# Optimization experiments

Measured on AMD Instinct MI355X. Metric: run time of the kernel, lower is better.

## Reference

```python
import jax, jax.numpy as jnp
import numpy as np

N = 100000
IN_C = 256
OUT_C = 256
E = 500000


def gcn_conv(x, W, b, edges):
    """PyG GCNConv: add self-loops, symmetric D^-1/2 (A+I) D^-1/2 normalization,
    then scatter-add of transformed source features into targets, plus bias."""
    n = x.shape[0]
    loop = jnp.arange(n, dtype=edges.dtype)
    row = jnp.concatenate([edges[0], loop])  # source
    col = jnp.concatenate([edges[1], loop])  # target
    deg = jax.ops.segment_sum(jnp.ones_like(col, dtype=x.dtype), col, num_segments=n)
    dis = jax.lax.rsqrt(deg)  # deg >= 1 after self-loops
    norm = dis[row] * dis[col]  # [E+n]
    h = x @ W  # [n, out]
    msg = h[row] * norm[:, None]  # gather + scale
    return jax.ops.segment_sum(msg, col, num_segments=n) + b


def setup_inputs() -> dict:
    key = jax.random.key(0)
    ks = jax.random.split(key, 24)
    x = jax.random.normal(ks[0], (N, IN_C), dtype=jnp.float32)
    edges00 = jax.random.randint(ks[1], (2, E), 0, N, dtype=jnp.int32)
    edges01 = jax.random.randint(ks[2], (2, E), 0, N, dtype=jnp.int32)
    edges10 = jax.random.randint(ks[3], (2, E), 0, N, dtype=jnp.int32)
    edges11 = jax.random.randint(ks[4], (2, E), 0, N, dtype=jnp.int32)
    t0 = (jax.random.uniform(ks[5], (N,)) > 0.5).astype(jnp.float32)
    t1 = 1.0 - t0
    scale = 1.0 / np.sqrt(IN_C)
    W1 = jax.random.normal(ks[6], (IN_C, OUT_C), dtype=jnp.float32) * scale
    W2 = jax.random.normal(ks[7], (IN_C, OUT_C), dtype=jnp.float32) * scale
    W3 = jax.random.normal(ks[8], (IN_C, OUT_C), dtype=jnp.float32) * scale
    W4 = jax.random.normal(ks[9], (IN_C, OUT_C), dtype=jnp.float32) * scale
    b1 = jnp.zeros((OUT_C,), jnp.float32)
    b2 = jnp.zeros((OUT_C,), jnp.float32)
    b3 = jnp.zeros((OUT_C,), jnp.float32)
    b4 = jnp.zeros((OUT_C,), jnp.float32)
    p0 = jax.random.normal(ks[10], (OUT_C,), dtype=jnp.float32)
    p1 = jax.random.normal(ks[11], (OUT_C,), dtype=jnp.float32)
    p2 = jax.random.normal(ks[12], (OUT_C,), dtype=jnp.float32)
    p3 = jax.random.normal(ks[13], (OUT_C,), dtype=jnp.float32)
    p4 = jax.random.normal(ks[14], (OUT_C,), dtype=jnp.float32)
    p5 = jax.random.normal(ks[15], (OUT_C,), dtype=jnp.float32)
    return dict(x=x, edges00=edges00, edges01=edges01, edges10=edges10, edges11=edges11,
                type0_idx=t0, type1_idx=t1,
                W1=W1, b1=b1, W2=W2, b2=b2, W3=W3, b3=b3, W4=W4, b4=b4,
                p0=p0, p1=p1, p2=p2, p3=p3, p4=p4, p5=p5)


def reference(x, edges00, edges01, edges10, edges11, type0_idx, type1_idx,
              W1, b1, W2, b2, W3, b3, W4, b4, p0, p1, p2, p3, p4, p5):
    # x0/x1: first feature column masked by node type, broadcast over out channels
    x0c = type0_idx * x[:, 0]  # [N]
    x1c = type1_idx * x[:, 0]
    x00 = gcn_conv(x, W1, b1, edges00)
    x01 = gcn_conv(x, W2, b2, edges01)
    x10 = gcn_conv(x, W3, b3, edges10)
    x11 = gcn_conv(x, W4, b4, edges11)
    out = (x0c[:, None] * p0 + x1c[:, None] * p1
           + x00 * p2 + x01 * p3 + x10 * p4 + x11 * p5)
    return out
```

## Files before the change

kernel.cpp:

```cpp
#include <hip/hip_runtime.h>


typedef __bf16 v8bf __attribute__((ext_vector_type(8)));
typedef float v4f __attribute__((ext_vector_type(4)));

__device__ __forceinline__ unsigned short f2bf(float f) {
  unsigned u = __float_as_uint(f);
  u += 0x7fffu + ((u >> 16) & 1u);
  return (unsigned short)(u >> 16);
}
__device__ __forceinline__ float bf2f(unsigned short s) {
  return __uint_as_float(((unsigned)s) << 16);
}

__global__ void lc_zero(int* __restrict__ p, int n) {
  int i = blockIdx.x * 256 + threadIdx.x;
  if (i < n) p[i] = 0;
}

__global__ void lc_hist(const int* __restrict__ e0, const int* __restrict__ e1,
                        const int* __restrict__ e2, const int* __restrict__ e3,
                        int* __restrict__ hist, int N, int E) {
  int e = blockIdx.x * 256 + threadIdx.x;
  if (e >= E) return;
  int k = blockIdx.y;
  const int* ed = (k == 0) ? e0 : (k == 1) ? e1 : (k == 2) ? e2 : e3;
  int col = ed[E + e];
  atomicAdd(&hist[k * N + col], 1);
}

__global__ void lc_dis(const int* __restrict__ hist, float* __restrict__ dis, int M) {
  int i = blockIdx.x * 256 + threadIdx.x;
  if (i < M) dis[i] = rsqrtf((float)(hist[i] + 1));
}

__global__ void lc_scan1(const int* __restrict__ in, int* __restrict__ outp,
                         int* __restrict__ bsum, int M) {
  __shared__ int tmp[256];
  int t = threadIdx.x, i = blockIdx.x * 256 + t;
  int v = (i < M) ? in[i] : 0;
  tmp[t] = v;
  __syncthreads();
  for (int off = 1; off < 256; off <<= 1) {
    int add = (t >= off) ? tmp[t - off] : 0;
    __syncthreads();
    tmp[t] += add;
    __syncthreads();
  }
  if (i < M) outp[i] = tmp[t] - v;
  if (t == 255) bsum[blockIdx.x] = tmp[255];
}

__global__ void lc_scan2(int* __restrict__ bsum, int nb) {
  __shared__ int tmp[256];
  __shared__ int carry_s;
  int t = threadIdx.x;
  if (t == 0) carry_s = 0;
  __syncthreads();
  for (int base = 0; base < nb; base += 256) {
    int i = base + t;
    int v = (i < nb) ? bsum[i] : 0;
    tmp[t] = v;
    __syncthreads();
    for (int off = 1; off < 256; off <<= 1) {
      int add = (t >= off) ? tmp[t - off] : 0;
      __syncthreads();
      tmp[t] += add;
      __syncthreads();
    }
    int carry = carry_s;
    int total = tmp[255];
    if (i < nb) bsum[i] = carry + tmp[t] - v;
    __syncthreads();
    if (t == 0) carry_s = carry + total;
    __syncthreads();
  }
}

__global__ void lc_scan3(int* __restrict__ rp, int* __restrict__ cursor,
                         const int* __restrict__ bsum, int M) {
  int i = blockIdx.x * 256 + threadIdx.x;
  if (i < M) {
    int v = rp[i] + bsum[blockIdx.x];
    rp[i] = v;
    cursor[i] = v;
  }
}

__global__ void lc_fill(const int* __restrict__ e0, const int* __restrict__ e1,
                        const int* __restrict__ e2, const int* __restrict__ e3,
                        int* __restrict__ cursor, const float* __restrict__ dis,
                        int2* __restrict__ payload, int N, int E) {
  int e = blockIdx.x * 256 + threadIdx.x;
  if (e >= E) return;
  int k = blockIdx.y;
  const int* ed = (k == 0) ? e0 : (k == 1) ? e1 : (k == 2) ? e2 : e3;
  int src = ed[e], col = ed[E + e];
  int pos = atomicAdd(&cursor[k * N + col], 1);
  float nrm = dis[k * N + src] * dis[k * N + col];
  payload[pos] = make_int2(src, __float_as_int(nrm));
}

__global__ void lc_bias(const float* __restrict__ b1, const float* __restrict__ b2,
                        const float* __restrict__ b3, const float* __restrict__ b4,
                        const float* __restrict__ p2, const float* __restrict__ p3,
                        const float* __restrict__ p4, const float* __restrict__ p5,
                        float* __restrict__ biasc) {
  int c = threadIdx.x;
  biasc[c] = b1[c] * p2[c] + b2[c] * p3[c] + b3[c] * p4[c] + b4[c] * p5[c];
}

__global__ void lc_prep(const float* __restrict__ W1, const float* __restrict__ W2,
                        const float* __restrict__ W3, const float* __restrict__ W4,
                        const float* __restrict__ p2, const float* __restrict__ p3,
                        const float* __restrict__ p4, const float* __restrict__ p5,
                        unsigned short* __restrict__ Wt) {
  int b = blockIdx.x;
  int k = b >> 8, co = b & 255;
  int kk = threadIdx.x;
  const float* W = (k == 0) ? W1 : (k == 1) ? W2 : (k == 2) ? W3 : W4;
  const float* p = (k == 0) ? p2 : (k == 1) ? p3 : (k == 2) ? p4 : p5;
  Wt[(size_t)co * 1024 + k * 256 + kk] = f2bf(W[kk * 256 + co] * p[co]);
}

__global__ void lc_cvt(const float4* __restrict__ x4, ushort4* __restrict__ xb4,
                       const float* __restrict__ t0, const float* __restrict__ t1,
                       float* __restrict__ m0, float* __restrict__ m1, int n4) {
  int i = blockIdx.x * 256 + threadIdx.x;
  if (i >= n4) return;
  float4 v = x4[i];
  ushort4 r;
  r.x = f2bf(v.x); r.y = f2bf(v.y); r.z = f2bf(v.z); r.w = f2bf(v.w);
  xb4[i] = r;
  if ((i & 63) == 0) {
    int n = i >> 6;
    float xc = v.x;
    m0[n] = t0[n] * xc;
    m1[n] = t1[n] * xc;
  }
}

#define GAT1(POS, A0, A1, A2, A3)                                       \
  do {                                                                  \
    int2 ee = payload[POS];                                             \
    ushort4 gg = *(const ushort4*)&xb[(size_t)ee.x * 256 + c];          \
    float nn = __int_as_float(ee.y);                                    \
    A0 += bf2f(gg.x) * nn;                                              \
    A1 += bf2f(gg.y) * nn;                                              \
    A2 += bf2f(gg.z) * nn;                                              \
    A3 += bf2f(gg.w) * nn;                                              \
  } while (0)

__global__ __launch_bounds__(512, 4) void lc_fused(
    const unsigned short* __restrict__ xb, const unsigned short* __restrict__ Wt,
    const int* __restrict__ rp, const int* __restrict__ hist,
    const float* __restrict__ dis, const int2* __restrict__ payload,
    float* __restrict__ out, int N,
    const float* __restrict__ m0, const float* __restrict__ m1,
    const float* __restrict__ p0, const float* __restrict__ p1,
    const float* __restrict__ biasc) {
  __shared__ alignas(16) unsigned short As[32 * 1024];
  const int t = threadIdx.x;
  const int w = t >> 6, lane = t & 63;
  const int quad = lane >> 4, l16 = lane & 15;
  const int n0 = blockIdx.x * 32;
  const int c = lane * 4;

  for (int pb = 0; pb < 16; pb += 2) {
    int pr = w * 16 + pb;
    int ln = pr >> 2;
    int k0 = pr & 3;
    int n = n0 + ln;
    if (n >= N) n = N - 1;
    int idx0 = k0 * N + n;
    int idx1 = idx0 + N;
    float d0 = dis[idx0], d1 = dis[idx1];
    float s0v = d0 * d0, s1v = d1 * d1;
    ushort4 hv = *(const ushort4*)&xb[(size_t)n * 256 + c];
    float x0 = bf2f(hv.x), x1 = bf2f(hv.y), x2 = bf2f(hv.z), x3 = bf2f(hv.w);
    float a0 = x0 * s0v, a1 = x1 * s0v, a2 = x2 * s0v, a3 = x3 * s0v;
    float b0 = x0 * s1v, b1 = x1 * s1v, b2 = x2 * s1v, b3 = x3 * s1v;
    int st0 = rp[idx0], cnt0 = hist[idx0];
    int st1 = rp[idx1], cnt1 = hist[idx1];
    int i0 = 0, i1 = 0;
    while (i0 + 4 <= cnt0 && i1 + 4 <= cnt1) {
      GAT1(st0 + i0 + 0, a0, a1, a2, a3);
      GAT1(st0 + i0 + 1, a0, a1, a2, a3);
      GAT1(st0 + i0 + 2, a0, a1, a2, a3);
      GAT1(st0 + i0 + 3, a0, a1, a2, a3);
      GAT1(st1 + i1 + 0, b0, b1, b2, b3);
      GAT1(st1 + i1 + 1, b0, b1, b2, b3);
      GAT1(st1 + i1 + 2, b0, b1, b2, b3);
      GAT1(st1 + i1 + 3, b0, b1, b2, b3);
      i0 += 4;
      i1 += 4;
    }
    for (; i0 + 4 <= cnt0; i0 += 4) {
      GAT1(st0 + i0 + 0, a0, a1, a2, a3);
      GAT1(st0 + i0 + 1, a0, a1, a2, a3);
      GAT1(st0 + i0 + 2, a0, a1, a2, a3);
      GAT1(st0 + i0 + 3, a0, a1, a2, a3);
    }
    for (; i0 < cnt0; ++i0) GAT1(st0 + i0, a0, a1, a2, a3);
    for (; i1 + 4 <= cnt1; i1 += 4) {
      GAT1(st1 + i1 + 0, b0, b1, b2, b3);
      GAT1(st1 + i1 + 1, b0, b1, b2, b3);
      GAT1(st1 + i1 + 2, b0, b1, b2, b3);
      GAT1(st1 + i1 + 3, b0, b1, b2, b3);
    }
    for (; i1 < cnt1; ++i1) GAT1(st1 + i1, b0, b1, b2, b3);

    unsigned swz = (unsigned)((ln & 7) << 3);
    ushort4 r0, r1;
    r0.x = f2bf(a0); r0.y = f2bf(a1); r0.z = f2bf(a2); r0.w = f2bf(a3);
    r1.x = f2bf(b0); r1.y = f2bf(b1); r1.z = f2bf(b2); r1.w = f2bf(b3);
    *(ushort4*)&As[(unsigned)ln * 1024 + (((unsigned)(k0 * 256 + c)) ^ swz)] = r0;
    *(ushort4*)&As[(unsigned)ln * 1024 + (((unsigned)((k0 + 1) * 256 + c)) ^ swz)] = r1;
  }
  __syncthreads();

  v4f acc[2][2];
#pragma unroll
  for (int mt = 0; mt < 2; mt++)
#pragma unroll
    for (int nt = 0; nt < 2; nt++) {
      v4f z = {0.f, 0.f, 0.f, 0.f};
      acc[mt][nt] = z;
    }

  const unsigned short* Bp = Wt + (size_t)(w * 32 + l16) * 1024 + quad * 8;
#pragma unroll 4
  for (int kk = 0; kk < 1024; kk += 32) {
    int eq = (kk + quad * 8) ^ ((l16 & 7) << 3);
    v8bf af0 = *(const v8bf*)&As[(unsigned)l16 * 1024 + eq];
    v8bf af1 = *(const v8bf*)&As[(unsigned)(l16 + 16) * 1024 + eq];
    v8bf bq0 = *(const v8bf*)&Bp[kk];
    v8bf bq1 = *(const v8bf*)&Bp[16384 + kk];
    acc[0][0] = __builtin_amdgcn_mfma_f32_16x16x32_bf16(af0, bq0, acc[0][0], 0, 0, 0);
    acc[0][1] = __builtin_amdgcn_mfma_f32_16x16x32_bf16(af0, bq1, acc[0][1], 0, 0, 0);
    acc[1][0] = __builtin_amdgcn_mfma_f32_16x16x32_bf16(af1, bq0, acc[1][0], 0, 0, 0);
    acc[1][1] = __builtin_amdgcn_mfma_f32_16x16x32_bf16(af1, bq1, acc[1][1], 0, 0, 0);
  }

  float pc0[2], pc1[2], bcv[2];
#pragma unroll
  for (int nt = 0; nt < 2; nt++) {
    int gcol = w * 32 + nt * 16 + l16;
    pc0[nt] = p0[gcol];
    pc1[nt] = p1[gcol];
    bcv[nt] = biasc[gcol];
  }
#pragma unroll
  for (int mt = 0; mt < 2; mt++)
#pragma unroll
    for (int r = 0; r < 4; r++) {
      int grow = n0 + mt * 16 + quad * 4 + r;
      if (grow >= N) continue;
      float m0v = m0[grow], m1v = m1[grow];
#pragma unroll
      for (int nt = 0; nt < 2; nt++) {
        int gcol = w * 32 + nt * 16 + l16;
        out[(size_t)grow * 256 + gcol] =
            acc[mt][nt][r] + m0v * pc0[nt] + m1v * pc1[nt] + bcv[nt];
      }
    }
}

extern "C" void kernel_launch(void* const* d_in, const int* in_sizes, int n_in,
                              void* d_out, int out_size, void* d_ws, size_t ws_size,
                              hipStream_t stream) {
  const float* x = (const float*)d_in[0];
  const int* e00 = (const int*)d_in[1];
  const int* e01 = (const int*)d_in[2];
  const int* e10 = (const int*)d_in[3];
  const int* e11 = (const int*)d_in[4];
  const float* t0 = (const float*)d_in[5];
  const float* t1 = (const float*)d_in[6];
  const float* W1 = (const float*)d_in[7];
  const float* b1 = (const float*)d_in[8];
  const float* W2 = (const float*)d_in[9];
  const float* b2 = (const float*)d_in[10];
  const float* W3 = (const float*)d_in[11];
  const float* b3 = (const float*)d_in[12];
  const float* W4 = (const float*)d_in[13];
  const float* b4 = (const float*)d_in[14];
  const float* p0 = (const float*)d_in[15];
  const float* p1 = (const float*)d_in[16];
  const float* p2 = (const float*)d_in[17];
  const float* p3 = (const float*)d_in[18];
  const float* p4 = (const float*)d_in[19];
  const float* p5 = (const float*)d_in[20];
  float* out = (float*)d_out;

  int N = in_sizes[0] / 256;
  int E = in_sizes[1] / 2;
  int M4 = 4 * N;
  int nb = (M4 + 255) / 256;

  char* wp = (char*)d_ws;
  auto carve = [&](size_t bytes) {
    void* r = (void*)wp;
    wp += (bytes + 255) & ~(size_t)255;
    return r;
  };
  unsigned short* xb = (unsigned short*)carve((size_t)N * 256 * 2);
  unsigned short* Wt = (unsigned short*)carve((size_t)256 * 1024 * 2);
  int* hist = (int*)carve((size_t)M4 * 4);
  float* dis = (float*)carve((size_t)M4 * 4);
  int* rp = (int*)carve((size_t)M4 * 4);
  int* cursor = (int*)carve((size_t)M4 * 4);
  int* bsum = (int*)carve((size_t)nb * 4);
  float* biasc = (float*)carve(256 * 4);
  float* m0 = (float*)carve((size_t)N * 4);
  float* m1 = (float*)carve((size_t)N * 4);
  int2* payload = (int2*)carve((size_t)4 * E * 8);

  int gE = (E + 255) / 256;
  int gM = (M4 + 255) / 256;

  lc_zero<<<gM, 256, 0, stream>>>(hist, M4);
  lc_hist<<<dim3(gE, 4), 256, 0, stream>>>(e00, e01, e10, e11, hist, N, E);
  lc_dis<<<gM, 256, 0, stream>>>(hist, dis, M4);
  lc_scan1<<<nb, 256, 0, stream>>>(hist, rp, bsum, M4);
  lc_scan2<<<1, 256, 0, stream>>>(bsum, nb);
  lc_scan3<<<nb, 256, 0, stream>>>(rp, cursor, bsum, M4);
  lc_fill<<<dim3(gE, 4), 256, 0, stream>>>(e00, e01, e10, e11, cursor, dis, payload, N, E);
  lc_bias<<<1, 256, 0, stream>>>(b1, b2, b3, b4, p2, p3, p4, p5, biasc);
  lc_prep<<<1024, 256, 0, stream>>>(W1, W2, W3, W4, p2, p3, p4, p5, Wt);
  lc_cvt<<<(N * 64 + 255) / 256, 256, 0, stream>>>((const float4*)x, (ushort4*)xb,
                                                   t0, t1, m0, m1, N * 64);

  lc_fused<<<dim3((N + 31) / 32), 512, 0, stream>>>(xb, Wt, rp, hist, dis, payload,
                                                    out, N, m0, m1, p0, p1, biasc);
}
```

Measured before the change: 821.3 us.

## Halve shared memory via two-phase K split and predicate gather loop for occupancy

The fused gather+GEMM kernel now processes the four edge-type relations in two halves of K=512. Each half is gathered into a 32KB shared tile and consumed by MFMA before the next, which halves LDS use and raises the launch-bounds occupancy target from 4 to 8. The gather loops are merged into one predicated loop over the longer neighbor list, clamping indices and zeroing weights to avoid divergent tail loops. Warps are also remapped to a 2x4 grid with 4 N-tiles each. Risks include an extra barrier, wasted predicated loads when the two degree counts differ, and register pressure under the tighter bound.

After: 1.033 ms. +25.7%, slower.

```diff
diff --git a/kernel.cpp b/kernel.cpp
--- a/kernel.cpp
+++ b/kernel.cpp
@@ -140,18 +140,19 @@
   }
 }
 
-#define GAT1(POS, A0, A1, A2, A3)                                       \
+#define GATC(BASE, POS, LIM, CNT, A0, A1, A2, A3)                       \
   do {                                                                  \
-    int2 ee = payload[POS];                                             \
+    int jj = ((POS) < (CNT)) ? (POS) : (LIM);                           \
+    int2 ee = payload[(BASE) + jj];                                     \
     ushort4 gg = *(const ushort4*)&xb[(size_t)ee.x * 256 + c];          \
-    float nn = __int_as_float(ee.y);                                    \
+    float nn = ((POS) < (CNT)) ? __int_as_float(ee.y) : 0.f;            \
     A0 += bf2f(gg.x) * nn;                                              \
     A1 += bf2f(gg.y) * nn;                                              \
     A2 += bf2f(gg.z) * nn;                                              \
     A3 += bf2f(gg.w) * nn;                                              \
   } while (0)
 
-__global__ __launch_bounds__(512, 4) void lc_fused(
+__global__ __launch_bounds__(512, 8) void lc_fused(
     const unsigned short* __restrict__ xb, const unsigned short* __restrict__ Wt,
     const int* __restrict__ rp, const int* __restrict__ hist,
     const float* __restrict__ dis, const int2* __restrict__ payload,
@@ -159,111 +160,96 @@
     const float* __restrict__ m0, const float* __restrict__ m1,
     const float* __restrict__ p0, const float* __restrict__ p1,
     const float* __restrict__ biasc) {
-  __shared__ alignas(16) unsigned short As[32 * 1024];
+  __shared__ alignas(16) unsigned short As[32 * 512];
   const int t = threadIdx.x;
   const int w = t >> 6, lane = t & 63;
   const int quad = lane >> 4, l16 = lane & 15;
+  const int wr = w >> 2, wc = w & 3;
   const int n0 = blockIdx.x * 32;
   const int c = lane * 4;
 
-  for (int pb = 0; pb < 16; pb += 2) {
-    int pr = w * 16 + pb;
-    int ln = pr >> 2;
-    int k0 = pr & 3;
-    int n = n0 + ln;
-    if (n >= N) n = N - 1;
-    int idx0 = k0 * N + n;
-    int idx1 = idx0 + N;
-    float d0 = dis[idx0], d1 = dis[idx1];
-    float s0v = d0 * d0, s1v = d1 * d1;
-    ushort4 hv = *(const ushort4*)&xb[(size_t)n * 256 + c];
-    float x0 = bf2f(hv.x), x1 = bf2f(hv.y), x2 = bf2f(hv.z), x3 = bf2f(hv.w);
-    float a0 = x0 * s0v, a1 = x1 * s0v, a2 = x2 * s0v, a3 = x3 * s0v;
-    float b0 = x0 * s1v, b1 = x1 * s1v, b2 = x2 * s1v, b3 = x3 * s1v;
-    int st0 = rp[idx0], cnt0 = hist[idx0];
-    int st1 = rp[idx1], cnt1 = hist[idx1];
-    int i0 = 0, i1 = 0;
-    while (i0 + 4 <= cnt0 && i1 + 4 <= cnt1) {
-      GAT1(st0 + i0 + 0, a0, a1, a2, a3);
-      GAT1(st0 + i0 + 1, a0, a1, a2, a3);
-      GAT1(st0 + i0 + 2, a0, a1, a2, a3);
-      GAT1(st0 + i0 + 3, a0, a1, a2, a3);
-      GAT1(st1 + i1 + 0, b0, b1, b2, b3);
-      GAT1(st1 + i1 + 1, b0, b1, b2, b3);
-      GAT1(st1 + i1 + 2, b0, b1, b2, b3);
-      GAT1(st1 + i1 + 3, b0, b1, b2, b3);
-      i0 += 4;
-      i1 += 4;
+  v4f acc[4];
+#pragma unroll
+  for (int nt = 0; nt < 4; nt++) {
+    v4f z = {0.f, 0.f, 0.f, 0.f};
+    acc[nt] = z;
+  }
+
+  for (int h = 0; h < 2; ++h) {
+    for (int rr = 0; rr < 4; ++rr) {
+      int ln = w * 4 + rr;
+      int n = n0 + ln;
+      if (n >= N) n = N - 1;
+      int idx0 = 2 * h * N + n;
+      int idx1 = idx0 + N;
+      float d0 = dis[idx0], d1 = dis[idx1];
+      float s0 = d0 * d0, s1 = d1 * d1;
+      ushort4 hv = *(const ushort4*)&xb[(size_t)n * 256 + c];
+      float x0 = bf2f(hv.x), x1 = bf2f(hv.y), x2 = bf2f(hv.z), x3 = bf2f(hv.w);
+      float a0 = x0 * s0, a1 = x1 * s0, a2 = x2 * s0, a3 = x3 * s0;
+      float u0 = x0 * s1, u1 = x1 * s1, u2 = x2 * s1, u3 = x3 * s1;
+      int st0 = rp[idx0], cnt0 = hist[idx0];
+      int st1 = rp[idx1], cnt1 = hist[idx1];
+      int bas0 = (cnt0 > 0) ? st0 : 0, lim0 = (cnt0 > 0) ? cnt0 - 1 : 0;
+      int bas1 = (cnt1 > 0) ? st1 : 0, lim1 = (cnt1 > 0) ? cnt1 - 1 : 0;
+      int cmax = (cnt0 > cnt1) ? cnt0 : cnt1;
+      for (int i = 0; i < cmax; i += 4) {
+        GATC(bas0, i + 0, lim0, cnt0, a0, a1, a2, a3);
+        GATC(bas0, i + 1, lim0, cnt0, a0, a1, a2, a3);
+        GATC(bas0, i + 2, lim0, cnt0, a0, a1, a2, a3);
+        GATC(bas0, i + 3, lim0, cnt0, a0, a1, a2, a3);
+        GATC(bas1, i + 0, lim1, cnt1, u0, u1, u2, u3);
+        GATC(bas1, i + 1, lim1, cnt1, u0, u1, u2, u3);
+        GATC(bas1, i + 2, lim1, cnt1, u0, u1, u2, u3);
+        GATC(bas1, i + 3, lim1, cnt1, u0, u1, u2, u3);
+      }
+      unsigned swz = (unsigned)((ln & 7) << 3);
+      ushort4 r0, r1;
+      r0.x = f2bf(a0); r0.y = f2bf(a1); r0.z = f2bf(a2); r0.w = f2bf(a3);
+      r1.x = f2bf(u0); r1.y = f2bf(u1); r1.z = f2bf(u2); r1.w = f2bf(u3);
+      *(ushort4*)&As[(unsigned)ln * 512 + (((unsigned)c) ^ swz)] = r0;
+      *(ushort4*)&As[(unsigned)ln * 512 + (((unsigned)(256 + c)) ^ swz)] = r1;
     }
-    for (; i0 + 4 <= cnt0; i0 += 4) {
-      GAT1(st0 + i0 + 0, a0, a1, a2, a3);
-      GAT1(st0 + i0 + 1, a0, a1, a2, a3);
-      GAT1(st0 + i0 + 2, a0, a1, a2, a3);
-      GAT1(st0 + i0 + 3, a0, a1, a2, a3);
+    __syncthreads();
+
+    {
+      const int rl = wr * 16 + l16;
+#pragma unroll 2
+      for (int kk = 0; kk < 512; kk += 32) {
+        int eq = (kk + quad * 8) ^ ((l16 & 7) << 3);
+        v8bf af = *(const v8bf*)&As[(unsigned)rl * 512 + eq];
+#pragma unroll
+        for (int nt = 0; nt < 4; nt++) {
+          const unsigned short* bp =
+              Wt + (size_t)(wc * 64 + nt * 16 + l16) * 1024 + h * 512 + kk + quad * 8;
+          v8bf bq = *(const v8bf*)bp;
+          acc[nt] = __builtin_amdgcn_mfma_f32_16x16x32_bf16(af, bq, acc[nt], 0, 0, 0);
+        }
+      }
     }
-    for (; i0 < cnt0; ++i0) GAT1(st0 + i0, a0, a1, a2, a3);
-    for (; i1 + 4 <= cnt1; i1 += 4) {
-      GAT1(st1 + i1 + 0, b0, b1, b2, b3);
-      GAT1(st1 + i1 + 1, b0, b1, b2, b3);
-      GAT1(st1 + i1 + 2, b0, b1, b2, b3);
-      GAT1(st1 + i1 + 3, b0, b1, b2, b3);
-    }
-    for (; i1 < cnt1; ++i1) GAT1(st1 + i1, b0, b1, b2, b3);
-
-    unsigned swz = (unsigned)((ln & 7) << 3);
-    ushort4 r0, r1;
-    r0.x = f2bf(a0); r0.y = f2bf(a1); r0.z = f2bf(a2); r0.w = f2bf(a3);
-    r1.x = f2bf(b0); r1.y = f2bf(b1); r1.z = f2bf(b2); r1.w = f2bf(b3);
-    *(ushort4*)&As[(unsigned)ln * 1024 + (((unsigned)(k0 * 256 + c)) ^ swz)] = r0;
-    *(ushort4*)&As[(unsigned)ln * 1024 + (((unsigned)((k0 + 1) * 256 + c)) ^ swz)] = r1;
-  }
-  __syncthreads();
-
-  v4f acc[2][2];
-#pragma unroll
-  for (int mt = 0; mt < 2; mt++)
-#pragma unroll
-    for (int nt = 0; nt < 2; nt++) {
-      v4f z = {0.f, 0.f, 0.f, 0.f};
-      acc[mt][nt] = z;
-    }
-
-  const unsigned short* Bp = Wt + (size_t)(w * 32 + l16) * 1024 + quad * 8;
-#pragma unroll 4
-  for (int kk = 0; kk < 1024; kk += 32) {
-    int eq = (kk + quad * 8) ^ ((l16 & 7) << 3);
-    v8bf af0 = *(const v8bf*)&As[(unsigned)l16 * 1024 + eq];
-    v8bf af1 = *(const v8bf*)&As[(unsigned)(l16 + 16) * 1024 + eq];
-    v8bf bq0 = *(const v8bf*)&Bp[kk];
-    v8bf bq1 = *(const v8bf*)&Bp[16384 + kk];
-    acc[0][0] = __builtin_amdgcn_mfma_f32_16x16x32_bf16(af0, bq0, acc[0][0], 0, 0, 0);
-    acc[0][1] = __builtin_amdgcn_mfma_f32_16x16x32_bf16(af0, bq1, acc[0][1], 0, 0, 0);
-    acc[1][0] = __builtin_amdgcn_mfma_f32_16x16x32_bf16(af1, bq0, acc[1][0], 0, 0, 0);
-    acc[1][1] = __builtin_amdgcn_mfma_f32_16x16x32_bf16(af1, bq1, acc[1][1], 0, 0, 0);
-  }
-
-  float pc0[2], pc1[2], bcv[2];
-#pragma unroll
-  for (int nt = 0; nt < 2; nt++) {
-    int gcol = w * 32 + nt * 16 + l16;
+    if (h == 0) __syncthreads();
+  }
+
+  float pc0[4], pc1[4], bcv[4];
+#pragma unroll
+  for (int nt = 0; nt < 4; nt++) {
+    int gcol = wc * 64 + nt * 16 + l16;
     pc0[nt] = p0[gcol];
     pc1[nt] = p1[gcol];
     bcv[nt] = biasc[gcol];
   }
 #pragma unroll
-  for (int mt = 0; mt < 2; mt++)
-#pragma unroll
-    for (int r = 0; r < 4; r++) {
-      int grow = n0 + mt * 16 + quad * 4 + r;
-      if (grow >= N) continue;
-      float m0v = m0[grow], m1v = m1[grow];
-#pragma unroll
-      for (int nt = 0; nt < 2; nt++) {
-        int gcol = w * 32 + nt * 16 + l16;
-        out[(size_t)grow * 256 + gcol] =
-            acc[mt][nt][r] + m0v * pc0[nt] + m1v * pc1[nt] + bcv[nt];
-      }
+  for (int r = 0; r < 4; r++) {
+    int grow = n0 + wr * 16 + quad * 4 + r;
+    if (grow >= N) continue;
+    float m0v = m0[grow], m1v = m1[grow];
+#pragma unroll
+    for (int nt = 0; nt < 4; nt++) {
+      int gcol = wc * 64 + nt * 16 + l16;
+      out[(size_t)grow * 256 + gcol] =
+          acc[nt][r] + m0v * pc0[nt] + m1v * pc1[nt] + bcv[nt];
     }
+  }
 }
 
 extern "C" void kernel_launch(void* const* d_in, const int* in_sizes, int n_in,
```

## Halve fused block row tile, raise occupancy, fold rsqrt into scan

Applied to the files above, without the earlier changes.

The fused gather+GEMM kernel now handles 16 nodes per block instead of 32. That halves LDS use to 32 KB and the accumulator registers, and launch bounds are raised to 6 blocks per CU to hide gather latency. Each warp now gathers one (node, edge-type) pair at a time with 4-way unrolled independent loads, replacing the interleaved two-pair loop. The degree rsqrt is computed inside the first scan kernel, which removes a separate launch. The cost is that the W tile is reloaded from global/L2 twice as often per node, and each MFMA A fragment is reused less.

Result: slower. 908.5 us (+10.6%).

```diff
diff --git a/kernel.cpp b/kernel.cpp
--- a/kernel.cpp
+++ b/kernel.cpp
@@ -29,16 +29,12 @@
   atomicAdd(&hist[k * N + col], 1);
 }
 
-__global__ void lc_dis(const int* __restrict__ hist, float* __restrict__ dis, int M) {
-  int i = blockIdx.x * 256 + threadIdx.x;
-  if (i < M) dis[i] = rsqrtf((float)(hist[i] + 1));
-}
-
 __global__ void lc_scan1(const int* __restrict__ in, int* __restrict__ outp,
-                         int* __restrict__ bsum, int M) {
+                         int* __restrict__ bsum, float* __restrict__ dis, int M) {
   __shared__ int tmp[256];
   int t = threadIdx.x, i = blockIdx.x * 256 + t;
   int v = (i < M) ? in[i] : 0;
+  if (i < M) dis[i] = rsqrtf((float)(v + 1));
   tmp[t] = v;
   __syncthreads();
   for (int off = 1; off < 256; off <<= 1) {
@@ -140,18 +136,7 @@
   }
 }
 
-#define GAT1(POS, A0, A1, A2, A3)                                       \
-  do {                                                                  \
-    int2 ee = payload[POS];                                             \
-    ushort4 gg = *(const ushort4*)&xb[(size_t)ee.x * 256 + c];          \
-    float nn = __int_as_float(ee.y);                                    \
-    A0 += bf2f(gg.x) * nn;                                              \
-    A1 += bf2f(gg.y) * nn;                                              \
-    A2 += bf2f(gg.z) * nn;                                              \
-    A3 += bf2f(gg.w) * nn;                                              \
-  } while (0)
-
-__global__ __launch_bounds__(512, 4) void lc_fused(
+__global__ __launch_bounds__(512, 6) void lc_fused(
     const unsigned short* __restrict__ xb, const unsigned short* __restrict__ Wt,
     const int* __restrict__ rp, const int* __restrict__ hist,
     const float* __restrict__ dis, const int2* __restrict__ payload,
@@ -159,87 +144,78 @@
     const float* __restrict__ m0, const float* __restrict__ m1,
     const float* __restrict__ p0, const float* __restrict__ p1,
     const float* __restrict__ biasc) {
-  __shared__ alignas(16) unsigned short As[32 * 1024];
+  __shared__ alignas(16) unsigned short As[16 * 1024];
   const int t = threadIdx.x;
   const int w = t >> 6, lane = t & 63;
   const int quad = lane >> 4, l16 = lane & 15;
-  const int n0 = blockIdx.x * 32;
+  const int n0 = blockIdx.x * 16;
   const int c = lane * 4;
 
-  for (int pb = 0; pb < 16; pb += 2) {
-    int pr = w * 16 + pb;
-    int ln = pr >> 2;
-    int k0 = pr & 3;
+  for (int j = 0; j < 8; ++j) {
+    int l = w * 8 + j;
+    int ln = l & 15, k = l >> 4;
     int n = n0 + ln;
     if (n >= N) n = N - 1;
-    int idx0 = k0 * N + n;
-    int idx1 = idx0 + N;
-    float d0 = dis[idx0], d1 = dis[idx1];
-    float s0v = d0 * d0, s1v = d1 * d1;
+    int idx = k * N + n;
+
+    float dn = dis[idx];
+    float s = dn * dn;
     ushort4 hv = *(const ushort4*)&xb[(size_t)n * 256 + c];
-    float x0 = bf2f(hv.x), x1 = bf2f(hv.y), x2 = bf2f(hv.z), x3 = bf2f(hv.w);
-    float a0 = x0 * s0v, a1 = x1 * s0v, a2 = x2 * s0v, a3 = x3 * s0v;
-    float b0 = x0 * s1v, b1 = x1 * s1v, b2 = x2 * s1v, b3 = x3 * s1v;
-    int st0 = rp[idx0], cnt0 = hist[idx0];
-    int st1 = rp[idx1], cnt1 = hist[idx1];
-    int i0 = 0, i1 = 0;
-    while (i0 + 4 <= cnt0 && i1 + 4 <= cnt1) {
-      GAT1(st0 + i0 + 0, a0, a1, a2, a3);
-      GAT1(st0 + i0 + 1, a0, a1, a2, a3);
-      GAT1(st0 + i0 + 2, a0, a1, a2, a3);
-      GAT1(st0 + i0 + 3, a0, a1, a2, a3);
-      GAT1(st1 + i1 + 0, b0, b1, b2, b3);
-      GAT1(st1 + i1 + 1, b0, b1, b2, b3);
-      GAT1(st1 + i1 + 2, b0, b1, b2, b3);
-      GAT1(st1 + i1 + 3, b0, b1, b2, b3);
-      i0 += 4;
-      i1 += 4;
+    float a0 = bf2f(hv.x) * s, a1 = bf2f(hv.y) * s;
+    float a2 = bf2f(hv.z) * s, a3 = bf2f(hv.w) * s;
+
+    int start = rp[idx];
+    int cnt = hist[idx];
+    int i = 0;
+    for (; i + 4 <= cnt; i += 4) {
+      int2 e0 = payload[start + i];
+      int2 e1 = payload[start + i + 1];
+      int2 e2 = payload[start + i + 2];
+      int2 e3 = payload[start + i + 3];
+      ushort4 g0 = *(const ushort4*)&xb[(size_t)e0.x * 256 + c];
+      ushort4 g1 = *(const ushort4*)&xb[(size_t)e1.x * 256 + c];
+      ushort4 g2 = *(const ushort4*)&xb[(size_t)e2.x * 256 + c];
+      ushort4 g3 = *(const ushort4*)&xb[(size_t)e3.x * 256 + c];
+      float n0v = __int_as_float(e0.y), n1v = __int_as_float(e1.y);
+      float n2v = __int_as_float(e2.y), n3v = __int_as_float(e3.y);
+      a0 += bf2f(g0.x) * n0v + bf2f(g1.x) * n1v + bf2f(g2.x) * n2v + bf2f(g3.x) * n3v;
+      a1 += bf2f(g0.y) * n0v + bf2f(g1.y) * n1v + bf2f(g2.y) * n2v + bf2f(g3.y) * n3v;
+      a2 += bf2f(g0.z) * n0v + bf2f(g1.z) * n1v + bf2f(g2.z) * n2v + bf2f(g3.z) * n3v;
+      a3 += bf2f(g0.w) * n0v + bf2f(g1.w) * n1v + bf2f(g2.w) * n2v + bf2f(g3.w) * n3v;
     }
-    for (; i0 + 4 <= cnt0; i0 += 4) {
-      GAT1(st0 + i0 + 0, a0, a1, a2, a3);
-      GAT1(st0 + i0 + 1, a0, a1, a2, a3);
-      GAT1(st0 + i0 + 2, a0, a1, a2, a3);
-      GAT1(st0 + i0 + 3, a0, a1, a2, a3);
+    for (; i < cnt; i++) {
+      int2 e0 = payload[start + i];
+      ushort4 g0 = *(const ushort4*)&xb[(size_t)e0.x * 256 + c];
+      float n0v = __int_as_float(e0.y);
+      a0 += bf2f(g0.x) * n0v;
+      a1 += bf2f(g0.y) * n0v;
+      a2 += bf2f(g0.z) * n0v;
+      a3 += bf2f(g0.w) * n0v;
     }
-    for (; i0 < cnt0; ++i0) GAT1(st0 + i0, a0, a1, a2, a3);
-    for (; i1 + 4 <= cnt1; i1 += 4) {
-      GAT1(st1 + i1 + 0, b0, b1, b2, b3);
-      GAT1(st1 + i1 + 1, b0, b1, b2, b3);
-      GAT1(st1 + i1 + 2, b0, b1, b2, b3);
-      GAT1(st1 + i1 + 3, b0, b1, b2, b3);
-    }
-    for (; i1 < cnt1; ++i1) GAT1(st1 + i1, b0, b1, b2, b3);
-
-    unsigned swz = (unsigned)((ln & 7) << 3);
-    ushort4 r0, r1;
-    r0.x = f2bf(a0); r0.y = f2bf(a1); r0.z = f2bf(a2); r0.w = f2bf(a3);
-    r1.x = f2bf(b0); r1.y = f2bf(b1); r1.z = f2bf(b2); r1.w = f2bf(b3);
-    *(ushort4*)&As[(unsigned)ln * 1024 + (((unsigned)(k0 * 256 + c)) ^ swz)] = r0;
-    *(ushort4*)&As[(unsigned)ln * 1024 + (((unsigned)((k0 + 1) * 256 + c)) ^ swz)] = r1;
+    ushort4 r;
+    r.x = f2bf(a0); r.y = f2bf(a1); r.z = f2bf(a2); r.w = f2bf(a3);
+    unsigned elem = ((unsigned)(k * 256 + c)) ^ ((unsigned)((ln & 7) << 3));
+    *(ushort4*)&As[(unsigned)ln * 1024 + elem] = r;
   }
   __syncthreads();
 
-  v4f acc[2][2];
+  v4f acc[2];
 #pragma unroll
-  for (int mt = 0; mt < 2; mt++)
-#pragma unroll
-    for (int nt = 0; nt < 2; nt++) {
-      v4f z = {0.f, 0.f, 0.f, 0.f};
-      acc[mt][nt] = z;
-    }
+  for (int nt = 0; nt < 2; nt++) {
+    v4f z = {0.f, 0.f, 0.f, 0.f};
+    acc[nt] = z;
+  }
 
   const unsigned short* Bp = Wt + (size_t)(w * 32 + l16) * 1024 + quad * 8;
+  const unsigned swzr = (unsigned)((l16 & 7) << 3);
 #pragma unroll 4
   for (int kk = 0; kk < 1024; kk += 32) {
-    int eq = (kk + quad * 8) ^ ((l16 & 7) << 3);
-    v8bf af0 = *(const v8bf*)&As[(unsigned)l16 * 1024 + eq];
-    v8bf af1 = *(const v8bf*)&As[(unsigned)(l16 + 16) * 1024 + eq];
+    unsigned eq = ((unsigned)(kk + quad * 8)) ^ swzr;
+    v8bf af = *(const v8bf*)&As[(unsigned)l16 * 1024 + eq];
     v8bf bq0 = *(const v8bf*)&Bp[kk];
     v8bf bq1 = *(const v8bf*)&Bp[16384 + kk];
-    acc[0][0] = __builtin_amdgcn_mfma_f32_16x16x32_bf16(af0, bq0, acc[0][0], 0, 0, 0);
-    acc[0][1] = __builtin_amdgcn_mfma_f32_16x16x32_bf16(af0, bq1, acc[0][1], 0, 0, 0);
-    acc[1][0] = __builtin_amdgcn_mfma_f32_16x16x32_bf16(af1, bq0, acc[1][0], 0, 0, 0);
-    acc[1][1] = __builtin_amdgcn_mfma_f32_16x16x32_bf16(af1, bq1, acc[1][1], 0, 0, 0);
+    acc[0] = __builtin_amdgcn_mfma_f32_16x16x32_bf16(af, bq0, acc[0], 0, 0, 0);
+    acc[1] = __builtin_amdgcn_mfma_f32_16x16x32_bf16(af, bq1, acc[1], 0, 0, 0);
   }
 
   float pc0[2], pc1[2], bcv[2];
@@ -251,19 +227,17 @@
     bcv[nt] = biasc[gcol];
   }
 #pragma unroll
-  for (int mt = 0; mt < 2; mt++)
+  for (int r = 0; r < 4; r++) {
+    int grow = n0 + quad * 4 + r;
+    if (grow >= N) continue;
+    float m0v = m0[grow], m1v = m1[grow];
 #pragma unroll
-    for (int r = 0; r < 4; r++) {
-      int grow = n0 + mt * 16 + quad * 4 + r;
-      if (grow >= N) continue;
-      float m0v = m0[grow], m1v = m1[grow];
-#pragma unroll
-      for (int nt = 0; nt < 2; nt++) {
-        int gcol = w * 32 + nt * 16 + l16;
-        out[(size_t)grow * 256 + gcol] =
-            acc[mt][nt][r] + m0v * pc0[nt] + m1v * pc1[nt] + bcv[nt];
-      }
+    for (int nt = 0; nt < 2; nt++) {
+      int gcol = w * 32 + nt * 16 + l16;
+      out[(size_t)grow * 256 + gcol] =
+          acc[nt][r] + m0v * pc0[nt] + m1v * pc1[nt] + bcv[nt];
     }
+  }
 }
 
 extern "C" void kernel_launch(void* const* d_in, const int* in_sizes, int n_in,
@@ -320,8 +294,7 @@
 
   lc_zero<<<gM, 256, 0, stream>>>(hist, M4);
   lc_hist<<<dim3(gE, 4), 256, 0, stream>>>(e00, e01, e10, e11, hist, N, E);
-  lc_dis<<<gM, 256, 0, stream>>>(hist, dis, M4);
-  lc_scan1<<<nb, 256, 0, stream>>>(hist, rp, bsum, M4);
+  lc_scan1<<<nb, 256, 0, stream>>>(hist, rp, bsum, dis, M4);
   lc_scan2<<<1, 256, 0, stream>>>(bsum, nb);
   lc_scan3<<<nb, 256, 0, stream>>>(rp, cursor, bsum, M4);
   lc_fill<<<dim3(gE, 4), 256, 0, stream>>>(e00, e01, e10, e11, cursor, dis, payload, N, E);
@@ -330,6 +303,6 @@
   lc_cvt<<<(N * 64 + 255) / 256, 256, 0, stream>>>((const float4*)x, (ushort4*)xb,
                                                    t0, t1, m0, m1, N * 64);
 
-  lc_fused<<<dim3((N + 31) / 32), 512, 0, stream>>>(xb, Wt, rp, hist, dis, payload,
+  lc_fused<<<dim3((N + 15) / 16), 512, 0, stream>>>(xb, Wt, rp, hist, dis, payload,
                                                     out, N, m0, m1, p0, p1, biasc);
 }
```
